# Kernel tuning notes

Measured on AMD Instinct MI355X. Metric: run time of the kernel, lower is better.

The kernel has to match this reference:

```python
import jax, jax.numpy as jnp
import numpy as np

WS, SS, NH = 7, 3, 3  # window_size, shift_size, num_heads


def window_partition(x, ws):
    B, H, W, C = x.shape
    x = x.reshape(B, H // ws, ws, W // ws, ws, C)
    return jnp.transpose(x, (0, 1, 3, 2, 4, 5)).reshape(-1, ws, ws, C)


def window_reverse(w, ws, H, W):
    B = w.shape[0] // (H * W // ws // ws)
    x = w.reshape(B, H // ws, W // ws, ws, ws, -1)
    return jnp.transpose(x, (0, 1, 3, 2, 4, 5)).reshape(B, H, W, -1)


def layernorm(x, scale, bias, eps=1e-6):
    mu = x.mean(-1, keepdims=True)
    var = ((x - mu) ** 2).mean(-1, keepdims=True)
    return (x - mu) * jax.lax.rsqrt(var + eps) * scale + bias


def make_attn_mask(Hp, Wp, ws, ss):
    # static (trace-time) shifted-window mask, (nW, N, N)
    img = np.zeros((1, Hp, Wp, 1), np.float32)
    cnt = 0
    for h in (slice(0, -ws), slice(-ws, -ss), slice(-ss, None)):
        for w in (slice(0, -ws), slice(-ws, -ss), slice(-ss, None)):
            img[:, h, w, :] = cnt
            cnt += 1
    mw = img.reshape(1, Hp // ws, ws, Wp // ws, ws, 1).transpose(0, 1, 3, 2, 4, 5).reshape(-1, ws * ws)
    am = mw[:, None, :] - mw[:, :, None]
    return np.where(am != 0, -100.0, 0.0).astype(np.float32)


def setup_inputs() -> dict:
    key = jax.random.key(0)
    ks = jax.random.split(key, 8)
    B, H, W, C = 4, 56, 56, 96
    s = lambda k, shape: jax.random.normal(k, shape, jnp.float32) * 0.02
    return {
        'x': jax.random.normal(ks[0], (B, H * W, C), jnp.float32),
        'Hp': H, 'Wp': W,
        'norm1_scale': jnp.ones((C,), jnp.float32), 'norm1_bias': jnp.zeros((C,), jnp.float32),
        'qkv_w': s(ks[1], (C, 3 * C)), 'qkv_b': jnp.zeros((3 * C,), jnp.float32),
        'proj_w': s(ks[2], (C, C)), 'proj_b': jnp.zeros((C,), jnp.float32),
        'tb_ln1_scale': jnp.ones((C,), jnp.float32), 'tb_ln1_bias': jnp.zeros((C,), jnp.float32),
        'tb_qkv_w': s(ks[3], (C, 3 * C)), 'tb_qkv_b': jnp.zeros((3 * C,), jnp.float32),
        'tb_out_w': s(ks[4], (C, C)), 'tb_out_b': jnp.zeros((C,), jnp.float32),
        'tb_ln2_scale': jnp.ones((C,), jnp.float32), 'tb_ln2_bias': jnp.zeros((C,), jnp.float32),
        'tb_fc1_w': s(ks[5], (C, 4 * C)), 'tb_fc1_b': jnp.zeros((4 * C,), jnp.float32),
        'tb_fc2_w': s(ks[6], (4 * C, C)), 'tb_fc2_b': jnp.zeros((C,), jnp.float32),
    }


def reference(x, Hp, Wp, norm1_scale, norm1_bias, qkv_w, qkv_b, proj_w, proj_b,
              tb_ln1_scale, tb_ln1_bias, tb_qkv_w, tb_qkv_b, tb_out_w, tb_out_b,
              tb_ln2_scale, tb_ln2_bias, tb_fc1_w, tb_fc1_b, tb_fc2_w, tb_fc2_b):
    ws, ss, nh = WS, SS, NH
    B, L, C = x.shape
    H, W = int(Hp), int(Wp)
    hd = C // nh
    shortcut = x
    h = layernorm(x, norm1_scale, norm1_bias).reshape(B, H, W, C)
    pad_r = (ws - W % ws) % ws
    pad_b = (ws - H % ws) % ws
    h = jnp.pad(h, ((0, 0), (0, pad_b), (0, pad_r), (0, 0)))
    Hpad, Wpad = H + pad_b, W + pad_r
    shifted = jnp.roll(h, (-ss, -ss), (1, 2))
    attn_mask = jnp.asarray(make_attn_mask(Hpad, Wpad, ws, ss))  # (nW, N, N)
    xw = window_partition(shifted, ws).reshape(-1, ws * ws, C)  # (B*nW, N, C)
    Bw, N, _ = xw.shape
    qkv = (xw @ qkv_w + qkv_b).reshape(Bw, N, 3, nh, hd).transpose(2, 0, 3, 1, 4)
    q, k, v = qkv[0], qkv[1], qkv[2]
    attn = jnp.einsum('bhnd,bhmd->bhnm', q, k) * hd ** -0.5
    nW = attn_mask.shape[0]
    attn = attn.reshape(Bw // nW, nW, nh, N, N) + attn_mask[None, :, None]
    attn = jax.nn.softmax(attn.reshape(-1, nh, N, N), axis=-1)
    out = jnp.einsum('bhnm,bhmd->bhnd', attn, v).transpose(0, 2, 1, 3).reshape(Bw, N, C)
    out = out @ proj_w + proj_b
    out = window_reverse(out.reshape(-1, ws, ws, C), ws, Hpad, Wpad)
    out = jnp.roll(out, (ss, ss), (1, 2))[:, :H, :W, :].reshape(B, H * W, C)
    x = shortcut + out
    # trailing pre-LN transformer block: global MHSA + MLP
    y = layernorm(x, tb_ln1_scale, tb_ln1_bias)
    qkv2 = (y @ tb_qkv_w + tb_qkv_b).reshape(B, L, 3, nh, hd).transpose(2, 0, 3, 1, 4)
    q2, k2, v2 = qkv2[0], qkv2[1], qkv2[2]
    a2 = jax.nn.softmax(jnp.einsum('bhnd,bhmd->bhnm', q2, k2) * hd ** -0.5, axis=-1)
    ao = jnp.einsum('bhnm,bhmd->bhnd', a2, v2).transpose(0, 2, 1, 3).reshape(B, L, C)
    x = x + (ao @ tb_out_w + tb_out_b)
    z = layernorm(x, tb_ln2_scale, tb_ln2_bias)
    z = jax.nn.gelu(z @ tb_fc1_w + tb_fc1_b) @ tb_fc2_w + tb_fc2_b
    x = x + z
    return (x, H, W)
```

## Files before the change

### kernel.cpp

```cpp
#include <hip/hip_runtime.h>
#include <hip/hip_bf16.h>

#define CD 96
#define LROW 3136
#define QSCALE 0.17677669529663687f
#define LOG2E 1.4426950408889634f
#define MASKLOG2 -144.26950408889634f

using f32x4 = __attribute__((ext_vector_type(4))) float;
using bf8   = __attribute__((ext_vector_type(8))) short;

__device__ __forceinline__ short f2bf(float f) {
  union { float f; unsigned u; } v; v.f = f;
  unsigned r = v.u + 0x7fffu + ((v.u >> 16) & 1u);
  return (short)(r >> 16);
}
__device__ __forceinline__ float bf2f(unsigned short s) {
  return __uint_as_float((unsigned)s << 16);
}
__device__ __forceinline__ unsigned pack_bf2(float lo, float hi) {
  return (__float_as_uint(hi) & 0xffff0000u) | (__float_as_uint(lo) >> 16);
}
__device__ __forceinline__ unsigned pack_bf2r(float lo, float hi) {
  return ((unsigned)(unsigned short)f2bf(hi) << 16) | (unsigned short)f2bf(lo);
}
__device__ __forceinline__ float fast_exp2(float x) {
  return __builtin_amdgcn_exp2f(x);
}

#define GLOAD_LDS16(src, dst) \
  __builtin_amdgcn_global_load_lds((const __attribute__((address_space(1))) void*)(src), \
                                   (__attribute__((address_space(3))) void*)(dst), 16, 0, 0)

__global__ __launch_bounds__(256) void ln_kernel(const float* __restrict__ x,
                                                 const float* __restrict__ g,
                                                 const float* __restrict__ b,
                                                 short* __restrict__ out, int rows) {
  int slot = threadIdx.x >> 5, l32 = threadIdx.x & 31;
  int row = blockIdx.x * 8 + slot;
  if (row >= rows) return;
  const float* xr = x + (size_t)row * CD + l32 * 3;
  float a0 = xr[0], a1 = xr[1], a2 = xr[2];
  float s = a0 + a1 + a2;
#pragma unroll
  for (int off = 16; off >= 1; off >>= 1) s += __shfl_xor(s, off, 32);
  float mu = s * (1.f / 96.f);
  float d0 = a0 - mu, d1 = a1 - mu, d2 = a2 - mu;
  float q = d0 * d0 + d1 * d1 + d2 * d2;
#pragma unroll
  for (int off = 16; off >= 1; off >>= 1) q += __shfl_xor(q, off, 32);
  float rstd = rsqrtf(q * (1.f / 96.f) + 1e-6f);
  int c0 = l32 * 3;
  short* orow = out + (size_t)row * CD + c0;
  orow[0] = f2bf(d0 * rstd * g[c0] + b[c0]);
  orow[1] = f2bf(d1 * rstd * g[c0 + 1] + b[c0 + 1]);
  orow[2] = f2bf(d2 * rstd * g[c0 + 2] + b[c0 + 2]);
}

__global__ __launch_bounds__(256) void cvt_all_kernel(
    const float* __restrict__ qkv2_w, const float* __restrict__ out_w,
    const float* __restrict__ fc1_w, const float* __restrict__ fc2_w,
    const float* __restrict__ qkv_w, const float* __restrict__ proj_w,
    short* __restrict__ dst,
    const int* __restrict__ Hp, const int* __restrict__ Wp,
    float* __restrict__ tail_out) {
  int idx = blockIdx.x * 256 + threadIdx.x;
  if (idx == 0) {
    tail_out[0] = (float)Hp[0];
    tail_out[1] = (float)Wp[0];
  }
  if (idx >= 165888) return;
  const float* W; int K, N, off;
  if (idx < 30720)       { W = qkv2_w; K = 96;  N = 288; off = idx; }
  else if (idx < 43008)  { W = out_w;  K = 96;  N = 96;  off = idx - 30720; }
  else if (idx < 79872)  { W = fc1_w;  K = 96;  N = 384; off = idx - 43008; }
  else if (idx < 129024) { W = fc2_w;  K = 384; N = 96;  off = idx - 79872; }
  else if (idx < 156672) { W = qkv_w;  K = 96;  N = 288; off = idx - 129024; }
  else                   { W = proj_w; K = 96;  N = 96;  off = idx - 156672; }
  int nr = off / K, kk = off - nr * K;
  float v = (nr < N) ? W[(size_t)kk * N + nr] : 0.f;
  dst[idx] = f2bf(v);
}

__global__ __launch_bounds__(512) void win_attn_kernel(
    const short* __restrict__ hb_in, const float* __restrict__ xin,
    const short* __restrict__ wwin, const float* __restrict__ qkv_b,
    const short* __restrict__ wproj, const float* __restrict__ proj_b,
    const float* __restrict__ ln1s, const float* __restrict__ ln1b,
    float* __restrict__ x1, short* __restrict__ hb2) {
  __shared__ __align__(16) short Xs[64][104];
  __shared__ __align__(16) short Qs[3][64][40];
  __shared__ __align__(16) short Ks[3][64][40];
  __shared__ __align__(16) short Vt[3][32][72];
  __shared__ __align__(16) short Os[64][104];
  __shared__ __align__(16) short Ptw[8][16][72];
  __shared__ int cnt[64];
  __shared__ int gidx[49];

  int tid = threadIdx.x, lane = tid & 63, wid = tid >> 6;
  int lr = lane & 15, lg = lane >> 4;
  int b = blockIdx.x >> 6, w64 = blockIdx.x & 63;
  int wr = w64 >> 3, wc = w64 & 7;

  if (tid < 64) {
    if (tid < 49) {
      int i = tid / 7, j = tid % 7;
      int sh = wr * 7 + i, sw = wc * 7 + j;
      int hr = (sh < 49) ? 0 : ((sh < 53) ? 1 : 2);
      int wreg = (sw < 49) ? 0 : ((sw < 53) ? 1 : 2);
      cnt[tid] = hr * 3 + wreg;
      gidx[tid] = ((sh + 3) % 56) * 56 + ((sw + 3) % 56);
    } else {
      cnt[tid] = -1;
    }
  }
  __syncthreads();

  for (int c = tid; c < 768; c += 512) {
    int row = c / 12, cc = c % 12;
    uint4 v = {0u, 0u, 0u, 0u};
    if (row < 49) v = *reinterpret_cast<const uint4*>(hb_in + ((size_t)b * LROW + gidx[row]) * 96 + cc * 8);
    *reinterpret_cast<uint4*>(&Xs[row][cc * 8]) = v;
  }
  __syncthreads();

  for (int nt = wid; nt < 18; nt += 8) {
    f32x4 acc[4];
#pragma unroll
    for (int mi = 0; mi < 4; ++mi) acc[mi] = (f32x4){0.f, 0.f, 0.f, 0.f};
#pragma unroll
    for (int kc = 0; kc < 3; ++kc) {
      bf8 bfr = *reinterpret_cast<const bf8*>(wwin + (size_t)(nt * 16 + lr) * 96 + kc * 32 + lg * 8);
#pragma unroll
      for (int mi = 0; mi < 4; ++mi) {
        bf8 afr = *reinterpret_cast<const bf8*>(&Xs[mi * 16 + lr][kc * 32 + lg * 8]);
        acc[mi] = __builtin_amdgcn_mfma_f32_16x16x32_bf16(afr, bfr, acc[mi], 0, 0, 0);
      }
    }
    int n = nt * 16 + lr;
    int sec = n / 96, within = n % 96;
    int hh = within >> 5, dd = within & 31;
    float bias = qkv_b[n];
#pragma unroll
    for (int mi = 0; mi < 4; ++mi)
#pragma unroll
      for (int r = 0; r < 4; ++r) {
        int mrow = mi * 16 + lg * 4 + r;
        float v = acc[mi][r] + bias;
        if (sec == 0)      Qs[hh][mrow][dd] = f2bf(v * (QSCALE * LOG2E));
        else if (sec == 1) Ks[hh][mrow][dd] = f2bf(v);
        else               Vt[hh][dd][mrow] = f2bf(v);
      }
  }
  __syncthreads();

  int cntkv[16];
#pragma unroll
  for (int t = 0; t < 4; ++t)
#pragma unroll
    for (int r = 0; r < 4; ++r) cntkv[t * 4 + r] = cnt[t * 16 + lg * 4 + r];

  for (int p = wid; p < 12; p += 8) {
    int h = p >> 2, qt = p & 3;
    bf8 qf = *reinterpret_cast<const bf8*>(&Qs[h][qt * 16 + lr][lg * 8]);
    int cq = cnt[qt * 16 + lr];
    f32x4 z = {0.f, 0.f, 0.f, 0.f};
    f32x4 St[4];
    __builtin_amdgcn_s_setprio(1);
#pragma unroll
    for (int t = 0; t < 4; ++t) {
      bf8 kf = *reinterpret_cast<const bf8*>(&Ks[h][t * 16 + lr][lg * 8]);
      St[t] = __builtin_amdgcn_mfma_f32_16x16x32_bf16(kf, qf, z, 0, 0, 0);
    }
    __builtin_amdgcn_s_setprio(0);
    float pr[4];
#pragma unroll
    for (int t = 0; t < 4; ++t) {
      float p0 = fast_exp2(St[t][0] + ((cq == cntkv[t * 4 + 0]) ? 0.f : MASKLOG2));
      float p1 = fast_exp2(St[t][1] + ((cq == cntkv[t * 4 + 1]) ? 0.f : MASKLOG2));
      float p2 = fast_exp2(St[t][2] + ((cq == cntkv[t * 4 + 2]) ? 0.f : MASKLOG2));
      float p3 = fast_exp2(St[t][3] + ((cq == cntkv[t * 4 + 3]) ? 0.f : MASKLOG2));
      St[t][0] = p0; St[t][1] = p1; St[t][2] = p2; St[t][3] = p3;
      pr[t] = (p0 + p1) + (p2 + p3);
    }
    float rs = (pr[0] + pr[1]) + (pr[2] + pr[3]);
    rs += __shfl_xor(rs, 16);
    rs += __shfl_xor(rs, 32);
    float inv = 1.f / rs;
#pragma unroll
    for (int t = 0; t < 4; ++t) {
      uint2 w;
      w.x = pack_bf2(St[t][0], St[t][1]);
      w.y = pack_bf2(St[t][2], St[t][3]);
      *reinterpret_cast<uint2*>(&Ptw[wid][lr][t * 16 + lg * 4]) = w;
    }
    f32x4 O0 = {0.f, 0.f, 0.f, 0.f}, O1 = {0.f, 0.f, 0.f, 0.f};
    __builtin_amdgcn_s_setprio(1);
#pragma unroll
    for (int c = 0; c < 2; ++c) {
      bf8 pbf = *reinterpret_cast<const bf8*>(&Ptw[wid][lr][c * 32 + lg * 8]);
      bf8 v0 = *reinterpret_cast<const bf8*>(&Vt[h][lr][c * 32 + lg * 8]);
      bf8 v1 = *reinterpret_cast<const bf8*>(&Vt[h][16 + lr][c * 32 + lg * 8]);
      O0 = __builtin_amdgcn_mfma_f32_16x16x32_bf16(v0, pbf, O0, 0, 0, 0);
      O1 = __builtin_amdgcn_mfma_f32_16x16x32_bf16(v1, pbf, O1, 0, 0, 0);
    }
    __builtin_amdgcn_s_setprio(0);
#pragma unroll
    for (int r = 0; r < 4; ++r) {
      Os[qt * 16 + lr][h * 32 + lg * 4 + r] = f2bf(O0[r] * inv);
      Os[qt * 16 + lr][h * 32 + 16 + lg * 4 + r] = f2bf(O1[r] * inv);
    }
  }
  __syncthreads();

  if (wid < 4) {
    int mt = wid;
    f32x4 acc[6];
#pragma unroll
    for (int nt = 0; nt < 6; ++nt) acc[nt] = (f32x4){0.f, 0.f, 0.f, 0.f};
#pragma unroll
    for (int kc = 0; kc < 3; ++kc) {
      bf8 afr = *reinterpret_cast<const bf8*>(&Os[mt * 16 + lr][kc * 32 + lg * 8]);
#pragma unroll
      for (int nt = 0; nt < 6; ++nt) {
        bf8 bfr = *reinterpret_cast<const bf8*>(wproj + (size_t)(nt * 16 + lr) * 96 + kc * 32 + lg * 8);
        acc[nt] = __builtin_amdgcn_mfma_f32_16x16x32_bf16(afr, bfr, acc[nt], 0, 0, 0);
      }
    }
    float pbv[6], gv[6], bv[6];
#pragma unroll
    for (int nt = 0; nt < 6; ++nt) {
      int col = nt * 16 + lr;
      pbv[nt] = proj_b[col];
      gv[nt] = ln1s[col];
      bv[nt] = ln1b[col];
    }
#pragma unroll
    for (int r = 0; r < 4; ++r) {
      int q = mt * 16 + lg * 4 + r;
      if (q >= 49) continue;
      size_t rb = ((size_t)b * LROW + gidx[q]) * CD;
      float v[6];
#pragma unroll
      for (int nt = 0; nt < 6; ++nt)
        v[nt] = acc[nt][r] + pbv[nt] + xin[rb + nt * 16 + lr];
      float s = ((v[0] + v[1]) + (v[2] + v[3])) + (v[4] + v[5]);
      s += __shfl_xor(s, 1); s += __shfl_xor(s, 2);
      s += __shfl_xor(s, 4); s += __shfl_xor(s, 8);
      float mu = s * (1.f / 96.f);
      float d[6];
      float qs = 0.f;
#pragma unroll
      for (int nt = 0; nt < 6; ++nt) { d[nt] = v[nt] - mu; qs += d[nt] * d[nt]; }
      qs += __shfl_xor(qs, 1); qs += __shfl_xor(qs, 2);
      qs += __shfl_xor(qs, 4); qs += __shfl_xor(qs, 8);
      float rstd = rsqrtf(qs * (1.f / 96.f) + 1e-6f);
#pragma unroll
      for (int nt = 0; nt < 6; ++nt) {
        x1[rb + nt * 16 + lr] = v[nt];
        hb2[rb + nt * 16 + lr] = f2bf(d[nt] * rstd * gv[nt] + bv[nt]);
      }
    }
  }
}

template <int MODE>
__global__ __launch_bounds__(256) void gemm_mfma_kernel(
    const short* __restrict__ A, const short* __restrict__ Bt,
    const float* __restrict__ bias, const float* __restrict__ res,
    void* __restrict__ outp, int M, int K, int N) {
  __shared__ __align__(16) short As[2][128 * 32];
  __shared__ __align__(16) short Bs[2][64 * 32];
  int tid = threadIdx.x, lane = tid & 63, wid = tid >> 6;
  int lr = lane & 15, lg = lane >> 4;
  int m0 = blockIdx.x * 128, n0 = blockIdx.y * 64;
  int nk = K >> 5;

  f32x4 acc[2][4];
#pragma unroll
  for (int i = 0; i < 2; ++i)
#pragma unroll
    for (int j = 0; j < 4; ++j) acc[i][j] = (f32x4){0.f, 0.f, 0.f, 0.f};

  auto stage = [&](int bf, int ks) {
    int k0 = ks * 32;
#pragma unroll
    for (int p = 0; p < 2; ++p) {
      int idx = tid + p * 256;
      GLOAD_LDS16(A + (size_t)(m0 + (idx >> 2)) * K + k0 + (idx & 3) * 8,
                  &As[bf][idx * 8]);
    }
    GLOAD_LDS16(Bt + (size_t)(n0 + (tid >> 2)) * K + k0 + (tid & 3) * 8,
                &Bs[bf][tid * 8]);
  };

  stage(0, 0);
  __syncthreads();
  int buf = 0;
  for (int ks = 0; ks < nk; ++ks) {
    if (ks + 1 < nk) stage(buf ^ 1, ks + 1);
    bf8 bfr[4], afr[2];
#pragma unroll
    for (int ni = 0; ni < 4; ++ni)
      bfr[ni] = *reinterpret_cast<const bf8*>(&Bs[buf][(ni * 16 + lr) * 32 + lg * 8]);
#pragma unroll
    for (int mi = 0; mi < 2; ++mi)
      afr[mi] = *reinterpret_cast<const bf8*>(&As[buf][(wid * 32 + mi * 16 + lr) * 32 + lg * 8]);
    __builtin_amdgcn_s_setprio(1);
#pragma unroll
    for (int mi = 0; mi < 2; ++mi)
#pragma unroll
      for (int ni = 0; ni < 4; ++ni)
        acc[mi][ni] = __builtin_amdgcn_mfma_f32_16x16x32_bf16(afr[mi], bfr[ni], acc[mi][ni], 0, 0, 0);
    __builtin_amdgcn_s_setprio(0);
    __syncthreads();
    buf ^= 1;
  }

#pragma unroll
  for (int mi = 0; mi < 2; ++mi)
#pragma unroll
    for (int ni = 0; ni < 4; ++ni)
#pragma unroll
      for (int r = 0; r < 4; ++r) {
        int mrow = m0 + wid * 32 + mi * 16 + lg * 4 + r;
        int n = n0 + ni * 16 + lr;
        if (n < N) {
          float v = acc[mi][ni][r] + bias[n];
          if (MODE == 0) {
            float t = tanhf(0.7978845608028654f * (v + 0.044715f * v * v * v));
            ((short*)outp)[(size_t)mrow * N + n] = f2bf(0.5f * v * (1.f + t));
          } else {
            v += res[(size_t)mrow * N + n];
            ((float*)outp)[(size_t)mrow * N + n] = v;
          }
        }
      }
}

__global__ __launch_bounds__(256) void gemm_out_ln_kernel(
    const short* __restrict__ A, const short* __restrict__ Bt,
    const float* __restrict__ bias, const float* __restrict__ res,
    const float* __restrict__ g2, const float* __restrict__ b2,
    float* __restrict__ x2, short* __restrict__ hb) {
  __shared__ __align__(16) short As[2][128 * 32];
  __shared__ __align__(16) short Bs[2][96 * 32];
  int tid = threadIdx.x, lane = tid & 63, wid = tid >> 6;
  int lr = lane & 15, lg = lane >> 4;
  int m0 = blockIdx.x * 128;
  const int K = 96;

  f32x4 acc[2][6];
#pragma unroll
  for (int i = 0; i < 2; ++i)
#pragma unroll
    for (int j = 0; j < 6; ++j) acc[i][j] = (f32x4){0.f, 0.f, 0.f, 0.f};

  auto stage = [&](int bf, int ks) {
    int k0 = ks * 32;
#pragma unroll
    for (int p = 0; p < 2; ++p) {
      int idx = tid + p * 256;
      GLOAD_LDS16(A + (size_t)(m0 + (idx >> 2)) * K + k0 + (idx & 3) * 8,
                  &As[bf][idx * 8]);
    }
    for (int l = tid; l < 384; l += 256) {
      GLOAD_LDS16(Bt + (size_t)(l >> 2) * K + k0 + (l & 3) * 8,
                  &Bs[bf][l * 8]);
    }
  };

  stage(0, 0);
  __syncthreads();
  int buf = 0;
  for (int ks = 0; ks < 3; ++ks) {
    if (ks + 1 < 3) stage(buf ^ 1, ks + 1);
    bf8 bfr[6], afr[2];
#pragma unroll
    for (int ni = 0; ni < 6; ++ni)
      bfr[ni] = *reinterpret_cast<const bf8*>(&Bs[buf][(ni * 16 + lr) * 32 + lg * 8]);
#pragma unroll
    for (int mi = 0; mi < 2; ++mi)
      afr[mi] = *reinterpret_cast<const bf8*>(&As[buf][(wid * 32 + mi * 16 + lr) * 32 + lg * 8]);
    __builtin_amdgcn_s_setprio(1);
#pragma unroll
    for (int mi = 0; mi < 2; ++mi)
#pragma unroll
      for (int ni = 0; ni < 6; ++ni)
        acc[mi][ni] = __builtin_amdgcn_mfma_f32_16x16x32_bf16(afr[mi], bfr[ni], acc[mi][ni], 0, 0, 0);
    __builtin_amdgcn_s_setprio(0);
    __syncthreads();
    buf ^= 1;
  }

  float bb[6], gv[6], bv[6];
#pragma unroll
  for (int ni = 0; ni < 6; ++ni) {
    int col = ni * 16 + lr;
    bb[ni] = bias[col];
    gv[ni] = g2[col];
    bv[ni] = b2[col];
  }
#pragma unroll
  for (int mi = 0; mi < 2; ++mi)
#pragma unroll
    for (int r = 0; r < 4; ++r) {
      int row = m0 + wid * 32 + mi * 16 + lg * 4 + r;
      size_t rb = (size_t)row * CD;
      float v[6];
#pragma unroll
      for (int ni = 0; ni < 6; ++ni)
        v[ni] = acc[mi][ni][r] + bb[ni] + res[rb + ni * 16 + lr];
      float s = ((v[0] + v[1]) + (v[2] + v[3])) + (v[4] + v[5]);
      s += __shfl_xor(s, 1); s += __shfl_xor(s, 2);
      s += __shfl_xor(s, 4); s += __shfl_xor(s, 8);
      float mu = s * (1.f / 96.f);
      float d[6];
      float qs = 0.f;
#pragma unroll
      for (int ni = 0; ni < 6; ++ni) { d[ni] = v[ni] - mu; qs += d[ni] * d[ni]; }
      qs += __shfl_xor(qs, 1); qs += __shfl_xor(qs, 2);
      qs += __shfl_xor(qs, 4); qs += __shfl_xor(qs, 8);
      float rstd = rsqrtf(qs * (1.f / 96.f) + 1e-6f);
#pragma unroll
      for (int ni = 0; ni < 6; ++ni) {
        x2[rb + ni * 16 + lr] = v[ni];
        hb[rb + ni * 16 + lr] = f2bf(d[ni] * rstd * gv[ni] + bv[ni]);
      }
    }
}

__global__ __launch_bounds__(256) void qkv_mfma_kernel(
    const short* __restrict__ A, const short* __restrict__ Bt,
    const float* __restrict__ bias,
    short* __restrict__ qb, short* __restrict__ kb, short* __restrict__ vtb) {
  __shared__ __align__(16) short As[2][128 * 32];
  __shared__ __align__(16) short Bs[2][64 * 32];
  int tid = threadIdx.x, lane = tid & 63, wid = tid >> 6;
  int lr = lane & 15, lg = lane >> 4;
  int m0 = blockIdx.x * 128, n0 = blockIdx.y * 64;
  const int K = 96;

  f32x4 acc[2][4];
#pragma unroll
  for (int i = 0; i < 2; ++i)
#pragma unroll
    for (int j = 0; j < 4; ++j) acc[i][j] = (f32x4){0.f, 0.f, 0.f, 0.f};

  auto stage = [&](int bf, int ks) {
    int k0 = ks * 32;
#pragma unroll
    for (int p = 0; p < 2; ++p) {
      int idx = tid + p * 256;
      GLOAD_LDS16(A + (size_t)(m0 + (idx >> 2)) * K + k0 + (idx & 3) * 8,
                  &As[bf][idx * 8]);
    }
    GLOAD_LDS16(Bt + (size_t)(n0 + (tid >> 2)) * K + k0 + (tid & 3) * 8,
                &Bs[bf][tid * 8]);
  };

  stage(0, 0);
  __syncthreads();
  int buf = 0;
  for (int ks = 0; ks < 3; ++ks) {
    if (ks + 1 < 3) stage(buf ^ 1, ks + 1);
    bf8 bfr[4], afr[2];
#pragma unroll
    for (int ni = 0; ni < 4; ++ni)
      bfr[ni] = *reinterpret_cast<const bf8*>(&Bs[buf][(ni * 16 + lr) * 32 + lg * 8]);
#pragma unroll
    for (int mi = 0; mi < 2; ++mi)
      afr[mi] = *reinterpret_cast<const bf8*>(&As[buf][(wid * 32 + mi * 16 + lr) * 32 + lg * 8]);
    __builtin_amdgcn_s_setprio(1);
#pragma unroll
    for (int mi = 0; mi < 2; ++mi)
#pragma unroll
      for (int ni = 0; ni < 4; ++ni)
        acc[mi][ni] = __builtin_amdgcn_mfma_f32_16x16x32_bf16(afr[mi], bfr[ni], acc[mi][ni], 0, 0, 0);
    __builtin_amdgcn_s_setprio(0);
    __syncthreads();
    buf ^= 1;
  }

#pragma unroll
  for (int mi = 0; mi < 2; ++mi)
#pragma unroll
    for (int ni = 0; ni < 4; ++ni)
#pragma unroll
      for (int r = 0; r < 4; ++r) {
        int mrow = m0 + wid * 32 + mi * 16 + lg * 4 + r;
        int n = n0 + ni * 16 + lr;
        if (n < 288) {
          float v = acc[mi][ni][r] + bias[n];
          int sec = n / 96, within = n % 96;
          int hh = within >> 5, dd = within & 31;
          int bb = mrow / LROW, nn = mrow - bb * LROW;
          size_t bh = (size_t)bb * 3 + hh;
          if (sec == 0)      qb[(bh * LROW + nn) * 32 + dd] = f2bf(v * (QSCALE * LOG2E));
          else if (sec == 1) kb[(bh * LROW + nn) * 32 + dd] = f2bf(v);
          else               vtb[(bh * 32 + dd) * LROW + nn] = f2bf(v);
        }
      }
}

__global__ __launch_bounds__(128) void flash_mfma_kernel(
    const short* __restrict__ qb, const short* __restrict__ kb,
    const short* __restrict__ vtb,
    short* __restrict__ pOb, float* __restrict__ pl) {
  __shared__ __align__(16) short Pt[2][2][16][72];
  int tid = threadIdx.x, lane = tid & 63, wid = tid >> 6;
  int lr = lane & 15, lg = lane >> 4;
  int bh = blockIdx.y, s = blockIdx.z;
  int q0 = blockIdx.x * 64 + wid * 32;
  const short* qbb = qb + (size_t)bh * LROW * 32;
  const short* kbase = kb + (size_t)bh * LROW * 32 + lr * 32 + lg * 8;
  const short* vbase = vtb + (size_t)bh * 32 * LROW + lr * LROW + lg * 8;

  bf8 qf0 = *reinterpret_cast<const bf8*>(qbb + (size_t)(q0 + lr) * 32 + lg * 8);
  bf8 qf1 = *reinterpret_cast<const bf8*>(qbb + (size_t)(q0 + 16 + lr) * 32 + lg * 8);

  f32x4 O00 = {0.f,0.f,0.f,0.f}, O01 = {0.f,0.f,0.f,0.f};
  f32x4 O10 = {0.f,0.f,0.f,0.f}, O11 = {0.f,0.f,0.f,0.f};
  float l0v = 0.f, l1v = 0.f;

  const int tbl[7] = {0, 9, 17, 25, 33, 41, 49};
  int t0 = tbl[s], t1 = tbl[s + 1];

  bf8 kA[4], vA[4], kB[4], vB[4];

  auto loadt = [&](bf8 (&Kf)[4], bf8 (&Vf)[4], int kt) {
    const short* kp = kbase + (size_t)kt * 2048;
#pragma unroll
    for (int t = 0; t < 4; ++t) Kf[t] = *reinterpret_cast<const bf8*>(kp + t * 512);
    const short* vp = vbase + kt * 64;
#pragma unroll
    for (int c = 0; c < 2; ++c) {
      Vf[c]     = *reinterpret_cast<const bf8*>(vp + c * 32);
      Vf[2 + c] = *reinterpret_cast<const bf8*>(vp + 16 * LROW + c * 32);
    }
  };

  auto body = [&](bf8 (&Kf)[4], bf8 (&Vf)[4]) {
    f32x4 z = {0.f, 0.f, 0.f, 0.f};
#pragma unroll
    for (int g = 0; g < 2; ++g) {
      bf8 qf = g ? qf1 : qf0;
      float& lgv = g ? l1v : l0v;
      f32x4 St[4];
      __builtin_amdgcn_s_setprio(1);
#pragma unroll
      for (int t = 0; t < 4; ++t)
        St[t] = __builtin_amdgcn_mfma_f32_16x16x32_bf16(Kf[t], qf, z, 0, 0, 0);
      __builtin_amdgcn_s_setprio(0);
      float pr[4];
#pragma unroll
      for (int t = 0; t < 4; ++t) {
        float p0 = fast_exp2(St[t][0]);
        float p1 = fast_exp2(St[t][1]);
        float p2 = fast_exp2(St[t][2]);
        float p3 = fast_exp2(St[t][3]);
        St[t][0] = p0; St[t][1] = p1; St[t][2] = p2; St[t][3] = p3;
        pr[t] = (p0 + p1) + (p2 + p3);
      }
      float rs = (pr[0] + pr[1]) + (pr[2] + pr[3]);
      rs += __shfl_xor(rs, 16);
      rs += __shfl_xor(rs, 32);
      lgv += rs;
#pragma unroll
      for (int t = 0; t < 4; ++t) {
        uint2 w;
        w.x = pack_bf2(St[t][0], St[t][1]);
        w.y = pack_bf2(St[t][2], St[t][3]);
        *reinterpret_cast<uint2*>(&Pt[wid][g][lr][t * 16 + lg * 4]) = w;
      }
    }
    __builtin_amdgcn_s_setprio(1);
#pragma unroll
    for (int g = 0; g < 2; ++g) {
      f32x4& Oh0 = g ? O10 : O00;
      f32x4& Oh1 = g ? O11 : O01;
#pragma unroll
      for (int c = 0; c < 2; ++c) {
        bf8 pbf = *reinterpret_cast<const bf8*>(&Pt[wid][g][lr][c * 32 + lg * 8]);
        Oh0 = __builtin_amdgcn_mfma_f32_16x16x32_bf16(Vf[c], pbf, Oh0, 0, 0, 0);
        Oh1 = __builtin_amdgcn_mfma_f32_16x16x32_bf16(Vf[2 + c], pbf, Oh1, 0, 0, 0);
      }
    }
    __builtin_amdgcn_s_setprio(0);
  };

  loadt(kA, vA, t0);
  int kt = t0;
  for (; kt + 2 <= t1 - 1; kt += 2) {
    loadt(kB, vB, kt + 1);
    body(kA, vA);
    loadt(kA, vA, kt + 2);
    body(kB, vB);
  }
  if (kt < t1 - 1) {
    loadt(kB, vB, kt + 1);
    body(kA, vA);
    body(kB, vB);
  } else {
    body(kA, vA);
  }

  size_t rbase = (size_t)(s * 12 + bh) * LROW;
  size_t r0 = (rbase + q0 + lr) * 32;
  size_t r1 = (rbase + q0 + 16 + lr) * 32;
  uint2 w;
  w.x = pack_bf2r(O00[0], O00[1]); w.y = pack_bf2r(O00[2], O00[3]);
  *reinterpret_cast<uint2*>(&pOb[r0 + lg * 4]) = w;
  w.x = pack_bf2r(O01[0], O01[1]); w.y = pack_bf2r(O01[2], O01[3]);
  *reinterpret_cast<uint2*>(&pOb[r0 + 16 + lg * 4]) = w;
  w.x = pack_bf2r(O10[0], O10[1]); w.y = pack_bf2r(O10[2], O10[3]);
  *reinterpret_cast<uint2*>(&pOb[r1 + lg * 4]) = w;
  w.x = pack_bf2r(O11[0], O11[1]); w.y = pack_bf2r(O11[2], O11[3]);
  *reinterpret_cast<uint2*>(&pOb[r1 + 16 + lg * 4]) = w;
  if (lg == 0) {
    pl[rbase + q0 + lr] = l0v;
    pl[rbase + q0 + 16 + lr] = l1v;
  }
}

__global__ __launch_bounds__(256) void flash_merge_kernel(
    const short* __restrict__ pOb, const float* __restrict__ pl,
    short* __restrict__ aob) {
  int idx = blockIdx.x * 256 + threadIdx.x;
  int d = idx & 31, row = idx >> 5;
  const int NR = 12 * LROW;
  float o = 0.f, l = 0.f;
#pragma unroll
  for (int s = 0; s < 6; ++s) {
    o += bf2f((unsigned short)pOb[(size_t)s * NR * 32 + idx]);
    l += pl[(size_t)s * NR + row];
  }
  int bh = row / LROW, q = row - bh * LROW;
  int b = bh / 3, h = bh - b * 3;
  aob[((size_t)b * LROW + q) * CD + h * 32 + d] = f2bf(o / l);
}

extern "C" void kernel_launch(void* const* d_in, const int* in_sizes, int n_in,
                              void* d_out, int out_size, void* d_ws, size_t ws_size,
                              hipStream_t stream) {
  const float* x      = (const float*)d_in[0];
  const int*   Hp     = (const int*)d_in[1];
  const int*   Wp     = (const int*)d_in[2];
  const float* n1s    = (const float*)d_in[3];
  const float* n1b    = (const float*)d_in[4];
  const float* qkv_w  = (const float*)d_in[5];
  const float* qkv_b  = (const float*)d_in[6];
  const float* proj_w = (const float*)d_in[7];
  const float* proj_b = (const float*)d_in[8];
  const float* ln1s   = (const float*)d_in[9];
  const float* ln1b   = (const float*)d_in[10];
  const float* qkv2_w = (const float*)d_in[11];
  const float* qkv2_b = (const float*)d_in[12];
  const float* out_w  = (const float*)d_in[13];
  const float* out_b  = (const float*)d_in[14];
  const float* ln2s   = (const float*)d_in[15];
  const float* ln2b   = (const float*)d_in[16];
  const float* fc1_w  = (const float*)d_in[17];
  const float* fc1_b  = (const float*)d_in[18];
  const float* fc2_w  = (const float*)d_in[19];
  const float* fc2_b  = (const float*)d_in[20];

  float* wsf = (float*)d_ws;
  const size_t U = (size_t)4 * LROW * CD;
  float* x1   = wsf;
  float* x2   = wsf + U;
  short* hb   = (short*)(wsf + 2 * U);
  short* tb   = (short*)(wsf + 2 * U + U / 2);
  short* qb   = (short*)(wsf + 4 * U + U / 2);
  short* kb   = qb + U;
  short* vtb  = kb + U;
  short* wall = (short*)(wsf + 6 * U);
  short* wqkv = wall;
  short* wout = wqkv + 320 * 96;
  short* wfc1 = wout + 128 * 96;
  short* wfc2 = wfc1 + 384 * 96;
  short* wwin = wfc2 + 128 * 384;
  short* wproj = wwin + 288 * 96;
  short* hb2  = (short*)(wsf + 6 * U + 82944);
  short* pOb  = (short*)(wsf + U);
  float* pl   = wsf + 4 * U;
  short* aob  = qb;
  float* outx = (float*)d_out;

  const int M = 4 * LROW;

  cvt_all_kernel<<<(165888 + 255) / 256, 256, 0, stream>>>(
      qkv2_w, out_w, fc1_w, fc2_w, qkv_w, proj_w, wall, Hp, Wp, outx + U);

  ln_kernel<<<M / 8, 256, 0, stream>>>(x, n1s, n1b, hb, M);
  win_attn_kernel<<<256, 512, 0, stream>>>(hb, x, wwin, qkv_b, wproj, proj_b,
                                           ln1s, ln1b, x1, hb2);
  qkv_mfma_kernel<<<dim3(M / 128, 5), 256, 0, stream>>>(hb2, wqkv, qkv2_b, qb, kb, vtb);
  flash_mfma_kernel<<<dim3(49, 12, 6), 128, 0, stream>>>(qb, kb, vtb, pOb, pl);
  flash_merge_kernel<<<12 * LROW * 32 / 256, 256, 0, stream>>>(pOb, pl, aob);
  gemm_out_ln_kernel<<<M / 128, 256, 0, stream>>>(aob, wout, out_b, x1, ln2s, ln2b, x2, hb);
  gemm_mfma_kernel<0><<<dim3(M / 128, 6), 256, 0, stream>>>(hb, wfc1, fc1_b, nullptr, tb, M, 96, 384);
  gemm_mfma_kernel<1><<<dim3(M / 128, 2), 256, 0, stream>>>(tb, wfc2, fc2_b, x2, outx, M, 384, 96);
}
```

Before: 118.1 us.

## Fuse flash merge into out-proj+LN kernel and fuse MLP fc1/fc2

Folds the split-KV flash merge into the output-projection+LayerNorm GEMM, so the merged attention output is built directly in LDS instead of round-tripping through global memory. Replaces the separate fc1 (GELU) and fc2 GEMMs with one MLP kernel that keeps the 384-wide hidden activation in LDS. GELU now uses an exp2/rcp form in place of tanhf. This removes two launches and the intermediate global buffers. In exchange, the MLP kernel reads its weights directly from global memory with large LDS use, and the merge step runs with only 384 work items per block, which may limit occupancy.

```diff
diff --git a/kernel.cpp b/kernel.cpp
--- a/kernel.cpp
+++ b/kernel.cpp
@@ -26,6 +26,11 @@
 }
 __device__ __forceinline__ float fast_exp2(float x) {
   return __builtin_amdgcn_exp2f(x);
+}
+__device__ __forceinline__ float gelu_f(float v) {
+  float u = 0.7978845608028654f * (v + 0.044715f * v * v * v);
+  float e = fast_exp2(u * 2.8853900817779268f);
+  return v * e * __builtin_amdgcn_rcpf(e + 1.f);
 }
 
 #define GLOAD_LDS16(src, dst) \
@@ -262,172 +267,6 @@
       }
     }
   }
-}
-
-template <int MODE>
-__global__ __launch_bounds__(256) void gemm_mfma_kernel(
-    const short* __restrict__ A, const short* __restrict__ Bt,
-    const float* __restrict__ bias, const float* __restrict__ res,
-    void* __restrict__ outp, int M, int K, int N) {
-  __shared__ __align__(16) short As[2][128 * 32];
-  __shared__ __align__(16) short Bs[2][64 * 32];
-  int tid = threadIdx.x, lane = tid & 63, wid = tid >> 6;
-  int lr = lane & 15, lg = lane >> 4;
-  int m0 = blockIdx.x * 128, n0 = blockIdx.y * 64;
-  int nk = K >> 5;
-
-  f32x4 acc[2][4];
-#pragma unroll
-  for (int i = 0; i < 2; ++i)
-#pragma unroll
-    for (int j = 0; j < 4; ++j) acc[i][j] = (f32x4){0.f, 0.f, 0.f, 0.f};
-
-  auto stage = [&](int bf, int ks) {
-    int k0 = ks * 32;
-#pragma unroll
-    for (int p = 0; p < 2; ++p) {
-      int idx = tid + p * 256;
-      GLOAD_LDS16(A + (size_t)(m0 + (idx >> 2)) * K + k0 + (idx & 3) * 8,
-                  &As[bf][idx * 8]);
-    }
-    GLOAD_LDS16(Bt + (size_t)(n0 + (tid >> 2)) * K + k0 + (tid & 3) * 8,
-                &Bs[bf][tid * 8]);
-  };
-
-  stage(0, 0);
-  __syncthreads();
-  int buf = 0;
-  for (int ks = 0; ks < nk; ++ks) {
-    if (ks + 1 < nk) stage(buf ^ 1, ks + 1);
-    bf8 bfr[4], afr[2];
-#pragma unroll
-    for (int ni = 0; ni < 4; ++ni)
-      bfr[ni] = *reinterpret_cast<const bf8*>(&Bs[buf][(ni * 16 + lr) * 32 + lg * 8]);
-#pragma unroll
-    for (int mi = 0; mi < 2; ++mi)
-      afr[mi] = *reinterpret_cast<const bf8*>(&As[buf][(wid * 32 + mi * 16 + lr) * 32 + lg * 8]);
-    __builtin_amdgcn_s_setprio(1);
-#pragma unroll
-    for (int mi = 0; mi < 2; ++mi)
-#pragma unroll
-      for (int ni = 0; ni < 4; ++ni)
-        acc[mi][ni] = __builtin_amdgcn_mfma_f32_16x16x32_bf16(afr[mi], bfr[ni], acc[mi][ni], 0, 0, 0);
-    __builtin_amdgcn_s_setprio(0);
-    __syncthreads();
-    buf ^= 1;
-  }
-
-#pragma unroll
-  for (int mi = 0; mi < 2; ++mi)
-#pragma unroll
-    for (int ni = 0; ni < 4; ++ni)
-#pragma unroll
-      for (int r = 0; r < 4; ++r) {
-        int mrow = m0 + wid * 32 + mi * 16 + lg * 4 + r;
-        int n = n0 + ni * 16 + lr;
-        if (n < N) {
-          float v = acc[mi][ni][r] + bias[n];
-          if (MODE == 0) {
-            float t = tanhf(0.7978845608028654f * (v + 0.044715f * v * v * v));
-            ((short*)outp)[(size_t)mrow * N + n] = f2bf(0.5f * v * (1.f + t));
-          } else {
-            v += res[(size_t)mrow * N + n];
-            ((float*)outp)[(size_t)mrow * N + n] = v;
-          }
-        }
-      }
-}
-
-__global__ __launch_bounds__(256) void gemm_out_ln_kernel(
-    const short* __restrict__ A, const short* __restrict__ Bt,
-    const float* __restrict__ bias, const float* __restrict__ res,
-    const float* __restrict__ g2, const float* __restrict__ b2,
-    float* __restrict__ x2, short* __restrict__ hb) {
-  __shared__ __align__(16) short As[2][128 * 32];
-  __shared__ __align__(16) short Bs[2][96 * 32];
-  int tid = threadIdx.x, lane = tid & 63, wid = tid >> 6;
-  int lr = lane & 15, lg = lane >> 4;
-  int m0 = blockIdx.x * 128;
-  const int K = 96;
-
-  f32x4 acc[2][6];
-#pragma unroll
-  for (int i = 0; i < 2; ++i)
-#pragma unroll
-    for (int j = 0; j < 6; ++j) acc[i][j] = (f32x4){0.f, 0.f, 0.f, 0.f};
-
-  auto stage = [&](int bf, int ks) {
-    int k0 = ks * 32;
-#pragma unroll
-    for (int p = 0; p < 2; ++p) {
-      int idx = tid + p * 256;
-      GLOAD_LDS16(A + (size_t)(m0 + (idx >> 2)) * K + k0 + (idx & 3) * 8,
-                  &As[bf][idx * 8]);
-    }
-    for (int l = tid; l < 384; l += 256) {
-      GLOAD_LDS16(Bt + (size_t)(l >> 2) * K + k0 + (l & 3) * 8,
-                  &Bs[bf][l * 8]);
-    }
-  };
-
-  stage(0, 0);
-  __syncthreads();
-  int buf = 0;
-  for (int ks = 0; ks < 3; ++ks) {
-    if (ks + 1 < 3) stage(buf ^ 1, ks + 1);
-    bf8 bfr[6], afr[2];
-#pragma unroll
-    for (int ni = 0; ni < 6; ++ni)
-      bfr[ni] = *reinterpret_cast<const bf8*>(&Bs[buf][(ni * 16 + lr) * 32 + lg * 8]);
-#pragma unroll
-    for (int mi = 0; mi < 2; ++mi)
-      afr[mi] = *reinterpret_cast<const bf8*>(&As[buf][(wid * 32 + mi * 16 + lr) * 32 + lg * 8]);
-    __builtin_amdgcn_s_setprio(1);
-#pragma unroll
-    for (int mi = 0; mi < 2; ++mi)
-#pragma unroll
-      for (int ni = 0; ni < 6; ++ni)
-        acc[mi][ni] = __builtin_amdgcn_mfma_f32_16x16x32_bf16(afr[mi], bfr[ni], acc[mi][ni], 0, 0, 0);
-    __builtin_amdgcn_s_setprio(0);
-    __syncthreads();
-    buf ^= 1;
-  }
-
-  float bb[6], gv[6], bv[6];
-#pragma unroll
-  for (int ni = 0; ni < 6; ++ni) {
-    int col = ni * 16 + lr;
-    bb[ni] = bias[col];
-    gv[ni] = g2[col];
-    bv[ni] = b2[col];
-  }
-#pragma unroll
-  for (int mi = 0; mi < 2; ++mi)
-#pragma unroll
-    for (int r = 0; r < 4; ++r) {
-      int row = m0 + wid * 32 + mi * 16 + lg * 4 + r;
-      size_t rb = (size_t)row * CD;
-      float v[6];
-#pragma unroll
-      for (int ni = 0; ni < 6; ++ni)
-        v[ni] = acc[mi][ni][r] + bb[ni] + res[rb + ni * 16 + lr];
-      float s = ((v[0] + v[1]) + (v[2] + v[3])) + (v[4] + v[5]);
-      s += __shfl_xor(s, 1); s += __shfl_xor(s, 2);
-      s += __shfl_xor(s, 4); s += __shfl_xor(s, 8);
-      float mu = s * (1.f / 96.f);
-      float d[6];
-      float qs = 0.f;
-#pragma unroll
-      for (int ni = 0; ni < 6; ++ni) { d[ni] = v[ni] - mu; qs += d[ni] * d[ni]; }
-      qs += __shfl_xor(qs, 1); qs += __shfl_xor(qs, 2);
-      qs += __shfl_xor(qs, 4); qs += __shfl_xor(qs, 8);
-      float rstd = rsqrtf(qs * (1.f / 96.f) + 1e-6f);
-#pragma unroll
-      for (int ni = 0; ni < 6; ++ni) {
-        x2[rb + ni * 16 + lr] = v[ni];
-        hb[rb + ni * 16 + lr] = f2bf(d[ni] * rstd * gv[ni] + bv[ni]);
-      }
-    }
 }
 
 __global__ __launch_bounds__(256) void qkv_mfma_kernel(
@@ -623,21 +462,217 @@
   }
 }
 
-__global__ __launch_bounds__(256) void flash_merge_kernel(
+__global__ __launch_bounds__(256) void gemm_out_merge_ln_kernel(
     const short* __restrict__ pOb, const float* __restrict__ pl,
-    short* __restrict__ aob) {
-  int idx = blockIdx.x * 256 + threadIdx.x;
-  int d = idx & 31, row = idx >> 5;
+    const short* __restrict__ Bt,
+    const float* __restrict__ bias, const float* __restrict__ res,
+    const float* __restrict__ g2, const float* __restrict__ b2,
+    float* __restrict__ x2, short* __restrict__ hb3) {
+  __shared__ __align__(16) short As[128][104];
+  __shared__ __align__(16) short Bs[2][96 * 32];
+  int tid = threadIdx.x, lane = tid & 63, wid = tid >> 6;
+  int lr = lane & 15, lg = lane >> 4;
+  int m0 = blockIdx.x * 128;
+  const int K = 96;
   const int NR = 12 * LROW;
-  float o = 0.f, l = 0.f;
-#pragma unroll
-  for (int s = 0; s < 6; ++s) {
-    o += bf2f((unsigned short)pOb[(size_t)s * NR * 32 + idx]);
-    l += pl[(size_t)s * NR + row];
-  }
-  int bh = row / LROW, q = row - bh * LROW;
-  int b = bh / 3, h = bh - b * 3;
-  aob[((size_t)b * LROW + q) * CD + h * 32 + d] = f2bf(o / l);
+
+  for (int pi = tid; pi < 384; pi += 256) {
+    int rloc = pi / 3, h = pi % 3;
+    int grow = m0 + rloc;
+    int bb = grow / LROW, q = grow - bb * LROW;
+    size_t pbase = ((size_t)(bb * 3 + h)) * LROW + q;
+    float l = 0.f;
+#pragma unroll
+    for (int s = 0; s < 6; ++s) l += pl[(size_t)s * NR + pbase];
+    float invl = 1.f / l;
+    float o[32];
+#pragma unroll
+    for (int d = 0; d < 32; ++d) o[d] = 0.f;
+#pragma unroll
+    for (int s = 0; s < 6; ++s) {
+      const uint4* p4 = reinterpret_cast<const uint4*>(pOb + ((size_t)s * NR + pbase) * 32);
+#pragma unroll
+      for (int u = 0; u < 4; ++u) {
+        uint4 v = p4[u];
+        unsigned wd0 = v.x, wd1 = v.y, wd2 = v.z, wd3 = v.w;
+        o[u*8+0] += __uint_as_float(wd0 << 16);
+        o[u*8+1] += __uint_as_float(wd0 & 0xffff0000u);
+        o[u*8+2] += __uint_as_float(wd1 << 16);
+        o[u*8+3] += __uint_as_float(wd1 & 0xffff0000u);
+        o[u*8+4] += __uint_as_float(wd2 << 16);
+        o[u*8+5] += __uint_as_float(wd2 & 0xffff0000u);
+        o[u*8+6] += __uint_as_float(wd3 << 16);
+        o[u*8+7] += __uint_as_float(wd3 & 0xffff0000u);
+      }
+    }
+    short* dst = &As[rloc][h * 32];
+#pragma unroll
+    for (int u2 = 0; u2 < 4; ++u2) {
+      uint4 w;
+      w.x = pack_bf2r(o[u2*8+0]*invl, o[u2*8+1]*invl);
+      w.y = pack_bf2r(o[u2*8+2]*invl, o[u2*8+3]*invl);
+      w.z = pack_bf2r(o[u2*8+4]*invl, o[u2*8+5]*invl);
+      w.w = pack_bf2r(o[u2*8+6]*invl, o[u2*8+7]*invl);
+      *reinterpret_cast<uint4*>(dst + u2 * 8) = w;
+    }
+  }
+
+  f32x4 acc[2][6];
+#pragma unroll
+  for (int i = 0; i < 2; ++i)
+#pragma unroll
+    for (int j = 0; j < 6; ++j) acc[i][j] = (f32x4){0.f, 0.f, 0.f, 0.f};
+
+  auto stageB = [&](int bf, int ks) {
+    int k0 = ks * 32;
+    for (int l = tid; l < 384; l += 256) {
+      GLOAD_LDS16(Bt + (size_t)(l >> 2) * K + k0 + (l & 3) * 8,
+                  &Bs[bf][l * 8]);
+    }
+  };
+
+  stageB(0, 0);
+  __syncthreads();
+  int buf = 0;
+  for (int ks = 0; ks < 3; ++ks) {
+    if (ks + 1 < 3) stageB(buf ^ 1, ks + 1);
+    bf8 bfr[6], afr[2];
+#pragma unroll
+    for (int ni = 0; ni < 6; ++ni)
+      bfr[ni] = *reinterpret_cast<const bf8*>(&Bs[buf][(ni * 16 + lr) * 32 + lg * 8]);
+#pragma unroll
+    for (int mi = 0; mi < 2; ++mi)
+      afr[mi] = *reinterpret_cast<const bf8*>(&As[wid * 32 + mi * 16 + lr][ks * 32 + lg * 8]);
+    __builtin_amdgcn_s_setprio(1);
+#pragma unroll
+    for (int mi = 0; mi < 2; ++mi)
+#pragma unroll
+      for (int ni = 0; ni < 6; ++ni)
+        acc[mi][ni] = __builtin_amdgcn_mfma_f32_16x16x32_bf16(afr[mi], bfr[ni], acc[mi][ni], 0, 0, 0);
+    __builtin_amdgcn_s_setprio(0);
+    __syncthreads();
+    buf ^= 1;
+  }
+
+  float bb[6], gv[6], bv[6];
+#pragma unroll
+  for (int ni = 0; ni < 6; ++ni) {
+    int col = ni * 16 + lr;
+    bb[ni] = bias[col];
+    gv[ni] = g2[col];
+    bv[ni] = b2[col];
+  }
+#pragma unroll
+  for (int mi = 0; mi < 2; ++mi)
+#pragma unroll
+    for (int r = 0; r < 4; ++r) {
+      int row = m0 + wid * 32 + mi * 16 + lg * 4 + r;
+      size_t rb = (size_t)row * CD;
+      float v[6];
+#pragma unroll
+      for (int ni = 0; ni < 6; ++ni)
+        v[ni] = acc[mi][ni][r] + bb[ni] + res[rb + ni * 16 + lr];
+      float s = ((v[0] + v[1]) + (v[2] + v[3])) + (v[4] + v[5]);
+      s += __shfl_xor(s, 1); s += __shfl_xor(s, 2);
+      s += __shfl_xor(s, 4); s += __shfl_xor(s, 8);
+      float mu = s * (1.f / 96.f);
+      float d[6];
+      float qs = 0.f;
+#pragma unroll
+      for (int ni = 0; ni < 6; ++ni) { d[ni] = v[ni] - mu; qs += d[ni] * d[ni]; }
+      qs += __shfl_xor(qs, 1); qs += __shfl_xor(qs, 2);
+      qs += __shfl_xor(qs, 4); qs += __shfl_xor(qs, 8);
+      float rstd = rsqrtf(qs * (1.f / 96.f) + 1e-6f);
+#pragma unroll
+      for (int ni = 0; ni < 6; ++ni) {
+        x2[rb + ni * 16 + lr] = v[ni];
+        hb3[rb + ni * 16 + lr] = f2bf(d[ni] * rstd * gv[ni] + bv[ni]);
+      }
+    }
+}
+
+__global__ __launch_bounds__(256) void mlp_kernel(
+    const short* __restrict__ hb3, const short* __restrict__ wfc1,
+    const float* __restrict__ fc1_b, const short* __restrict__ wfc2,
+    const float* __restrict__ fc2_b, const float* __restrict__ resid,
+    float* __restrict__ outx) {
+  __shared__ __align__(16) short Ah[64][104];
+  __shared__ __align__(16) short T[64][392];
+  int tid = threadIdx.x, lane = tid & 63, wid = tid >> 6;
+  int lr = lane & 15, lg = lane >> 4;
+  int m0 = blockIdx.x * 64;
+
+  for (int i = tid; i < 768; i += 256) {
+    int row = i / 12, c8 = i % 12;
+    uint4 v = *reinterpret_cast<const uint4*>(hb3 + (size_t)(m0 + row) * 96 + c8 * 8);
+    *reinterpret_cast<uint4*>(&Ah[row][c8 * 8]) = v;
+  }
+  __syncthreads();
+
+  {
+    f32x4 acc[4][6];
+#pragma unroll
+    for (int i = 0; i < 4; ++i)
+#pragma unroll
+      for (int j = 0; j < 6; ++j) acc[i][j] = (f32x4){0.f, 0.f, 0.f, 0.f};
+#pragma unroll
+    for (int kc = 0; kc < 3; ++kc) {
+      bf8 bfr[6], afr[4];
+#pragma unroll
+      for (int nt = 0; nt < 6; ++nt)
+        bfr[nt] = *reinterpret_cast<const bf8*>(wfc1 + (size_t)(wid * 96 + nt * 16 + lr) * 96 + kc * 32 + lg * 8);
+#pragma unroll
+      for (int mi = 0; mi < 4; ++mi)
+        afr[mi] = *reinterpret_cast<const bf8*>(&Ah[mi * 16 + lr][kc * 32 + lg * 8]);
+      __builtin_amdgcn_s_setprio(1);
+#pragma unroll
+      for (int mi = 0; mi < 4; ++mi)
+#pragma unroll
+        for (int nt = 0; nt < 6; ++nt)
+          acc[mi][nt] = __builtin_amdgcn_mfma_f32_16x16x32_bf16(afr[mi], bfr[nt], acc[mi][nt], 0, 0, 0);
+      __builtin_amdgcn_s_setprio(0);
+    }
+#pragma unroll
+    for (int nt = 0; nt < 6; ++nt) {
+      float b1 = fc1_b[wid * 96 + nt * 16 + lr];
+      int col = wid * 96 + nt * 16 + lr;
+#pragma unroll
+      for (int mi = 0; mi < 4; ++mi)
+#pragma unroll
+        for (int r = 0; r < 4; ++r)
+          T[mi * 16 + lg * 4 + r][col] = f2bf(gelu_f(acc[mi][nt][r] + b1));
+    }
+  }
+  __syncthreads();
+
+  {
+    f32x4 a2[6];
+#pragma unroll
+    for (int j = 0; j < 6; ++j) a2[j] = (f32x4){0.f, 0.f, 0.f, 0.f};
+#pragma unroll
+    for (int kc = 0; kc < 12; ++kc) {
+      bf8 afr2 = *reinterpret_cast<const bf8*>(&T[wid * 16 + lr][kc * 32 + lg * 8]);
+      bf8 bfr2[6];
+#pragma unroll
+      for (int nt = 0; nt < 6; ++nt)
+        bfr2[nt] = *reinterpret_cast<const bf8*>(wfc2 + (size_t)(nt * 16 + lr) * 384 + kc * 32 + lg * 8);
+      __builtin_amdgcn_s_setprio(1);
+#pragma unroll
+      for (int nt = 0; nt < 6; ++nt)
+        a2[nt] = __builtin_amdgcn_mfma_f32_16x16x32_bf16(afr2, bfr2[nt], a2[nt], 0, 0, 0);
+      __builtin_amdgcn_s_setprio(0);
+    }
+#pragma unroll
+    for (int nt = 0; nt < 6; ++nt) {
+      float b2v = fc2_b[nt * 16 + lr];
+#pragma unroll
+      for (int r = 0; r < 4; ++r) {
+        int row = m0 + wid * 16 + lg * 4 + r;
+        size_t idx = (size_t)row * CD + nt * 16 + lr;
+        outx[idx] = a2[nt][r] + b2v + resid[idx];
+      }
+    }
+  }
 }
 
 extern "C" void kernel_launch(void* const* d_in, const int* in_sizes, int n_in,
@@ -668,9 +703,7 @@
   float* wsf = (float*)d_ws;
   const size_t U = (size_t)4 * LROW * CD;
   float* x1   = wsf;
-  float* x2   = wsf + U;
   short* hb   = (short*)(wsf + 2 * U);
-  short* tb   = (short*)(wsf + 2 * U + U / 2);
   short* qb   = (short*)(wsf + 4 * U + U / 2);
   short* kb   = qb + U;
   short* vtb  = kb + U;
@@ -684,7 +717,8 @@
   short* hb2  = (short*)(wsf + 6 * U + 82944);
   short* pOb  = (short*)(wsf + U);
   float* pl   = wsf + 4 * U;
-  short* aob  = qb;
+  float* x2f  = (float*)qb;
+  short* hb3  = vtb;
   float* outx = (float*)d_out;
 
   const int M = 4 * LROW;
@@ -697,8 +731,7 @@
                                            ln1s, ln1b, x1, hb2);
   qkv_mfma_kernel<<<dim3(M / 128, 5), 256, 0, stream>>>(hb2, wqkv, qkv2_b, qb, kb, vtb);
   flash_mfma_kernel<<<dim3(49, 12, 6), 128, 0, stream>>>(qb, kb, vtb, pOb, pl);
-  flash_merge_kernel<<<12 * LROW * 32 / 256, 256, 0, stream>>>(pOb, pl, aob);
-  gemm_out_ln_kernel<<<M / 128, 256, 0, stream>>>(aob, wout, out_b, x1, ln2s, ln2b, x2, hb);
-  gemm_mfma_kernel<0><<<dim3(M / 128, 6), 256, 0, stream>>>(hb, wfc1, fc1_b, nullptr, tb, M, 96, 384);
-  gemm_mfma_kernel<1><<<dim3(M / 128, 2), 256, 0, stream>>>(tb, wfc2, fc2_b, x2, outx, M, 384, 96);
-}
+  gemm_out_merge_ln_kernel<<<M / 128, 256, 0, stream>>>(pOb, pl, wout, out_b, x1,
+                                                        ln2s, ln2b, x2f, hb3);
+  mlp_kernel<<<M / 64, 256, 0, stream>>>(hb3, wfc1, fc1_b, wfc2, fc2_b, x2f, outx);
+}
```

Result: faster. 114.9 us (-2.7%).
